# Kernel optimization log

Measured on AMD Instinct MI355X. Metric: run time of the kernel, lower is better.

Reference implementation:

```python
import jax, jax.numpy as jnp
import numpy as np

EMBED_DIM = 1024
NUM_HEADS = 16
SCALE = (EMBED_DIM // NUM_HEADS) ** -0.5  # 0.125


def setup_inputs() -> dict:
    key = jax.random.key(0)
    ks = jax.random.split(key, 9)
    B, S, E = 4, 2048, EMBED_DIM
    std = E ** -0.5
    x = jax.random.normal(ks[0], (B, S, E), dtype=jnp.float32)
    Wq = jax.random.normal(ks[1], (E, E), dtype=jnp.float32) * std
    bq = jax.random.normal(ks[2], (E,), dtype=jnp.float32) * 0.01
    Wk = jax.random.normal(ks[3], (E, E), dtype=jnp.float32) * std
    bk = jax.random.normal(ks[4], (E,), dtype=jnp.float32) * 0.01
    Wv = jax.random.normal(ks[5], (E, E), dtype=jnp.float32) * std
    bv = jax.random.normal(ks[6], (E,), dtype=jnp.float32) * 0.01
    Wo = jax.random.normal(ks[7], (E, E), dtype=jnp.float32) * std
    bo = jax.random.normal(ks[8], (E,), dtype=jnp.float32) * 0.01
    return {"x": x, "Wq": Wq, "bq": bq, "Wk": Wk, "bk": bk,
            "Wv": Wv, "bv": bv, "Wo": Wo, "bo": bo}


def reference(x, Wq, bq, Wk, bk, Wv, bv, Wo, bo):
    # torch nn.Linear: y = x @ W.T + b
    q = jnp.einsum('bse,fe->bsf', x, Wq) + bq   # [B,S,E]
    k = jnp.einsum('bse,fe->bsf', x, Wk) + bk
    v = jnp.einsum('bse,fe->bsf', x, Wv) + bv
    # Bilinear (no softmax) attention: scores = (Q K^T) * scale
    scores = jnp.einsum('bse,bte->bst', q, k) * SCALE  # [B,S,S]
    out = jnp.einsum('bst,bte->bse', scores, v)        # [B,S,E]
    return jnp.einsum('bse,fe->bsf', out, Wo) + bo
```

## Files before the change

### kernel.cpp

```cpp
#include <hip/hip_runtime.h>
#include <stdint.h>

typedef __bf16 bf16_t;
typedef __bf16 bf16x8 __attribute__((ext_vector_type(8)));
typedef __bf16 bf16x4 __attribute__((ext_vector_type(4)));
typedef float floatx4 __attribute__((ext_vector_type(4)));

__device__ __forceinline__ void async_copy16(const bf16_t* g, bf16_t* l) {
  __builtin_amdgcn_global_load_lds(
      (const __attribute__((address_space(1))) void*)g,
      (__attribute__((address_space(3))) void*)l, 16, 0, 0);
}

struct CvtSeg { const float* s; bf16_t* d; long n; };
struct CvtArgs { CvtSeg seg[5]; };

__global__ void cvt_multi(CvtArgs a) {
  CvtSeg sg = a.seg[blockIdx.y];
#pragma unroll
  for (int it = 0; it < 4; it++) {
    long i = (((long)blockIdx.x + (long)it * 2048) * 256 + threadIdx.x) * 4;
    if (i < sg.n) {
      float4 f = *(const float4*)(sg.s + i);
      bf16x4 o;
      o[0] = (bf16_t)f.x; o[1] = (bf16_t)f.y; o[2] = (bf16_t)f.z; o[3] = (bf16_t)f.w;
      *(bf16x4*)(sg.d + i) = o;
    }
  }
}

__global__ __launch_bounds__(256, 2) void qkv3(
    const bf16_t* __restrict__ xb,
    const bf16_t* __restrict__ Wq, const bf16_t* __restrict__ Wk, const bf16_t* __restrict__ Wv,
    const float* __restrict__ bq, const float* __restrict__ bk, const float* __restrict__ bv,
    bf16_t* __restrict__ qout, bf16_t* __restrict__ kT, bf16_t* __restrict__ vT) {
  __shared__ bf16_t As[2 * 4096];
  __shared__ bf16_t Bsh[3][2 * 4096];
  const int L = blockIdx.x;
  const int V = (L & 7) * 64 + (L >> 3);
  const int batch = V >> 7;
  const int rr_   = V & 127;
  const int n0 = (rr_ & 7) * 128;
  const int m0 = (rr_ >> 3) * 128;

  const int tid = threadIdx.x, lane = tid & 63, w = tid >> 6;
  const int wr = w >> 1, wc = w & 1, quad = lane >> 4, lm = lane & 15;
  const int ar = lane >> 2;
  const int ak = (((lane & 3) ^ ((ar >> 1) & 3))) * 8;
  const int swz = (lm >> 1) & 3;

  const bf16_t* ag0 = xb + (long)batch * (2048L * 1024) + (long)(m0 + w * 16 + ar) * 1024 + ak;
  const bf16_t* ag1 = ag0 + 64L * 1024;
  const bf16_t* Wp[3] = {Wq, Wk, Wv};
  const bf16_t* bg0[3];
  const bf16_t* bg1[3];
#pragma unroll
  for (int p = 0; p < 3; p++) {
    bg0[p] = Wp[p] + (long)(n0 + w * 16 + ar) * 1024 + ak;
    bg1[p] = bg0[p] + 64L * 1024;
  }

  floatx4 acc[3][4][4];
#pragma unroll
  for (int p = 0; p < 3; p++)
#pragma unroll
    for (int r = 0; r < 4; r++)
#pragma unroll
      for (int c = 0; c < 4; c++)
        acc[p][r][c] = (floatx4){0.f, 0.f, 0.f, 0.f};

  {
    bf16_t* la = As + w * 512;
    async_copy16(ag0, la);
    async_copy16(ag1, la + 2048);
#pragma unroll
    for (int p = 0; p < 3; p++) {
      bf16_t* lb = Bsh[p] + w * 512;
      async_copy16(bg0[p], lb);
      async_copy16(bg1[p], lb + 2048);
    }
  }
  for (int i = 0; i < 32; i++) {
    __syncthreads();
    if (i + 1 < 32) {
      const int buf = (i + 1) & 1, k0 = (i + 1) * 32;
      bf16_t* la = As + buf * 4096 + w * 512;
      async_copy16(ag0 + k0, la);
      async_copy16(ag1 + k0, la + 2048);
#pragma unroll
      for (int p = 0; p < 3; p++) {
        bf16_t* lb = Bsh[p] + buf * 4096 + w * 512;
        async_copy16(bg0[p] + k0, lb);
        async_copy16(bg1[p] + k0, lb + 2048);
      }
    }
    const bf16_t* Ar = As + (i & 1) * 4096;
    bf16x8 afr[4];
#pragma unroll
    for (int r = 0; r < 4; r++)
      afr[r] = *(const bf16x8*)&Ar[(wr * 64 + r * 16 + lm) * 32 + (quad ^ swz) * 8];
#pragma unroll
    for (int p = 0; p < 3; p++) {
      const bf16_t* Br = Bsh[p] + (i & 1) * 4096;
      bf16x8 bfr[4];
#pragma unroll
      for (int c = 0; c < 4; c++)
        bfr[c] = *(const bf16x8*)&Br[(wc * 64 + c * 16 + lm) * 32 + (quad ^ swz) * 8];
#pragma unroll
      for (int r = 0; r < 4; r++)
#pragma unroll
        for (int c = 0; c < 4; c++)
          acc[p][r][c] = __builtin_amdgcn_mfma_f32_16x16x32_bf16(afr[r], bfr[c], acc[p][r][c], 0, 0, 0);
    }
  }

  const int rowBase = m0 + wr * 64, colBase = n0 + wc * 64;
  {
    bf16_t* C = qout + (long)batch * (2048L * 1024);
#pragma unroll
    for (int r = 0; r < 4; r++) {
      const int row = rowBase + r * 16 + quad * 4;
#pragma unroll
      for (int c = 0; c < 4; c++) {
        const int col = colBase + c * 16 + lm;
        const float bv_ = bq[col];
#pragma unroll
        for (int i = 0; i < 4; i++)
          C[(long)(row + i) * 1024 + col] = (bf16_t)(acc[0][r][c][i] + bv_);
      }
    }
  }
#pragma unroll
  for (int p = 1; p < 3; p++) {
    bf16_t* C = ((p == 1) ? kT : vT) + (long)batch * (1024L * 2048);
    const float* bias = (p == 1) ? bk : bv;
#pragma unroll
    for (int r = 0; r < 4; r++) {
      const int row = rowBase + r * 16 + quad * 4;
#pragma unroll
      for (int c = 0; c < 4; c++) {
        const int col = colBase + c * 16 + lm;
        const float bv_ = bias[col];
        bf16x4 pk;
#pragma unroll
        for (int i = 0; i < 4; i++) pk[i] = (bf16_t)(acc[p][r][c][i] + bv_);
        *(bf16x4*)(C + (long)col * 2048 + row) = pk;
      }
    }
  }
}

template<int OUT_MODE, bool HAS_BIAS, int TOTAL, int BPZ>
__global__ __launch_bounds__(256) void gemm_wp(
    const bf16_t* __restrict__ A, const bf16_t* __restrict__ B,
    void* __restrict__ C, const float* __restrict__ bias,
    int lda, int ldb, int nk, long sA, long sB, long sC, int ldc, float alpha) {
  __shared__ bf16_t Ls[4 * 8192];
  const int L = blockIdx.x;
  const int V = (L & 7) * (TOTAL / 8) + (L >> 3);
  const int batch = V / BPZ;
  const int r_ = V % BPZ;
  const int n0 = (r_ & 7) * 128;
  const int m0 = (r_ >> 3) * 128;

  const int tid = threadIdx.x, lane = tid & 63, w = tid >> 6;
  const int wr = w >> 1, wc = w & 1, quad = lane >> 4, lm = lane & 15;
  const int ar = lane >> 2;
  const int ak = (((lane & 3) ^ ((ar >> 1) & 3))) * 8;
  const int swz = (lm >> 1) & 3;

  bf16_t* Lw = Ls + w * 8192;
  const bf16_t* Ab = A + (long)batch * sA;
  const bf16_t* Bb = B + (long)batch * sB;
  const bf16_t* agA = Ab + (long)(m0 + wr * 64 + ar) * lda + ak;
  const bf16_t* agB = Bb + (long)(n0 + wc * 64 + ar) * ldb + ak;

  auto STAGE = [&](int t, int b) {
    const int k0 = t * 32;
    bf16_t* d = Lw + b * 4096;
#pragma unroll
    for (int j = 0; j < 4; j++)
      async_copy16(agA + (long)j * 16 * lda + k0, d + j * 512);
#pragma unroll
    for (int j = 0; j < 4; j++)
      async_copy16(agB + (long)j * 16 * ldb + k0, d + 2048 + j * 512);
  };

  floatx4 acc[4][4];
#pragma unroll
  for (int r = 0; r < 4; r++)
#pragma unroll
    for (int c = 0; c < 4; c++) acc[r][c] = (floatx4){0.f, 0.f, 0.f, 0.f};

  STAGE(0, 0);
  for (int i = 0; i < nk; i++) {
    if (i + 1 < nk) {
      STAGE(i + 1, (i + 1) & 1);
      asm volatile("s_waitcnt vmcnt(8)" ::: "memory");
    } else {
      asm volatile("s_waitcnt vmcnt(0)" ::: "memory");
    }
    const bf16_t* Aw = Lw + (i & 1) * 4096;
    const bf16_t* Bw = Aw + 2048;
    bf16x8 afr[4], bfr[4];
#pragma unroll
    for (int r = 0; r < 4; r++)
      afr[r] = *(const bf16x8*)&Aw[(r * 16 + lm) * 32 + (quad ^ swz) * 8];
#pragma unroll
    for (int c = 0; c < 4; c++)
      bfr[c] = *(const bf16x8*)&Bw[(c * 16 + lm) * 32 + (quad ^ swz) * 8];
#pragma unroll
    for (int r = 0; r < 4; r++)
#pragma unroll
      for (int c = 0; c < 4; c++)
        acc[r][c] = __builtin_amdgcn_mfma_f32_16x16x32_bf16(afr[r], bfr[c], acc[r][c], 0, 0, 0);
  }

  const int rowBase = m0 + wr * 64, colBase = n0 + wc * 64;
  if (OUT_MODE == 0) {
    bf16_t* Cb = (bf16_t*)C + (long)batch * sC;
#pragma unroll
    for (int r = 0; r < 4; r++) {
      const int row = rowBase + r * 16 + quad * 4;
#pragma unroll
      for (int c = 0; c < 4; c++) {
        const int col = colBase + c * 16 + lm;
        const float bv_ = HAS_BIAS ? bias[col] : 0.f;
#pragma unroll
        for (int i = 0; i < 4; i++)
          Cb[(long)(row + i) * ldc + col] = (bf16_t)(acc[r][c][i] * alpha + bv_);
      }
    }
  } else {
    float* Cf = (float*)C + (long)batch * sC;
#pragma unroll
    for (int r = 0; r < 4; r++) {
      const int row = rowBase + r * 16 + quad * 4;
#pragma unroll
      for (int c = 0; c < 4; c++) {
        const int col = colBase + c * 16 + lm;
        const float bv_ = HAS_BIAS ? bias[col] : 0.f;
#pragma unroll
        for (int i = 0; i < 4; i++)
          Cf[(long)(row + i) * ldc + col] = acc[r][c][i] * alpha + bv_;
      }
    }
  }
}

extern "C" void kernel_launch(void* const* d_in, const int* in_sizes, int n_in,
                              void* d_out, int out_size, void* d_ws, size_t ws_size,
                              hipStream_t stream) {
  const float* x  = (const float*)d_in[0];
  const float* Wq = (const float*)d_in[1];
  const float* bq = (const float*)d_in[2];
  const float* Wk = (const float*)d_in[3];
  const float* bk = (const float*)d_in[4];
  const float* Wv = (const float*)d_in[5];
  const float* bv = (const float*)d_in[6];
  const float* Wo = (const float*)d_in[7];
  const float* bo = (const float*)d_in[8];
  float* out = (float*)d_out;

  const long NX = 8192L * 1024;
  const long NW = 1024L * 1024;

  bf16_t* ws  = (bf16_t*)d_ws;
  bf16_t* xb  = ws;
  bf16_t* Wqb = xb + NX;
  bf16_t* Wkb = Wqb + NW;
  bf16_t* Wvb = Wkb + NW;
  bf16_t* Wob = Wvb + NW;
  bf16_t* qb  = Wob + NW;
  bf16_t* kT  = qb + NX;
  bf16_t* vT  = kT + NX;
  bf16_t* MtTb = xb;
  bf16_t* Gb   = vT;

  CvtArgs ca;
  ca.seg[0] = {x,  xb,  NX};
  ca.seg[1] = {Wq, Wqb, NW};
  ca.seg[2] = {Wk, Wkb, NW};
  ca.seg[3] = {Wv, Wvb, NW};
  ca.seg[4] = {Wo, Wob, NW};
  cvt_multi<<<dim3(2048, 5), 256, 0, stream>>>(ca);

  qkv3<<<dim3(512), 256, 0, stream>>>(xb, Wqb, Wkb, Wvb, bq, bk, bv, qb, kT, vT);

  gemm_wp<0, false, 256, 64><<<dim3(256), 256, 0, stream>>>(
      kT, vT, MtTb, nullptr, 2048, 2048, 64,
      1024L * 2048, 1024L * 2048, 1024L * 1024, 1024, 0.125f);

  gemm_wp<0, false, 256, 64><<<dim3(256), 256, 0, stream>>>(
      Wob, MtTb, Gb, nullptr, 1024, 1024, 32,
      0L, 1024L * 1024, 1024L * 1024, 1024, 1.0f);

  gemm_wp<2, true, 512, 128><<<dim3(512), 256, 0, stream>>>(
      qb, Gb, out, bo, 1024, 1024, 32,
      2048L * 1024, 1024L * 1024, 2048L * 1024, 1024, 1.0f);
}
```

Measured before the change: 231.7 us.

## Fuse three tail GEMMs into one persistent kernel with grid-wide atomic barriers

Replaces the three separate GEMM launches (K^T V, Wo·M, Q·G) with a single persistent 256-block kernel that runs each stage as a tile loop and separates the stages with atomic-counter grid barriers. The barrier counters are zeroed by the conversion kernel. The aim is to remove two kernel launch gaps and the tail idle time between dependent GEMMs. In exchange it relies on all 256 blocks being co-resident and adds spin-wait barrier overhead. The last stage now runs two tiles per block instead of using 512 blocks, and the shared memory allocation grows.

Result: slower. 275.5 us (+18.9%).

```diff
diff --git a/kernel.cpp b/kernel.cpp
--- a/kernel.cpp
+++ b/kernel.cpp
@@ -13,9 +13,11 @@
 }
 
 struct CvtSeg { const float* s; bf16_t* d; long n; };
-struct CvtArgs { CvtSeg seg[5]; };
+struct CvtArgs { CvtSeg seg[5]; unsigned* sync; };
 
 __global__ void cvt_multi(CvtArgs a) {
+  if (blockIdx.x == 0 && blockIdx.y == 0 && threadIdx.x < 8)
+    a.sync[threadIdx.x] = 0u;
   CvtSeg sg = a.seg[blockIdx.y];
 #pragma unroll
   for (int it = 0; it < 4; it++) {
@@ -150,30 +152,13 @@
   }
 }
 
-template<int OUT_MODE, bool HAS_BIAS, int TOTAL, int BPZ>
-__global__ __launch_bounds__(256) void gemm_wp(
-    const bf16_t* __restrict__ A, const bf16_t* __restrict__ B,
-    void* __restrict__ C, const float* __restrict__ bias,
-    int lda, int ldb, int nk, long sA, long sB, long sC, int ldc, float alpha) {
-  __shared__ bf16_t Ls[4 * 8192];
-  const int L = blockIdx.x;
-  const int V = (L & 7) * (TOTAL / 8) + (L >> 3);
-  const int batch = V / BPZ;
-  const int r_ = V % BPZ;
-  const int n0 = (r_ & 7) * 128;
-  const int m0 = (r_ >> 3) * 128;
-
-  const int tid = threadIdx.x, lane = tid & 63, w = tid >> 6;
-  const int wr = w >> 1, wc = w & 1, quad = lane >> 4, lm = lane & 15;
-  const int ar = lane >> 2;
-  const int ak = (((lane & 3) ^ ((ar >> 1) & 3))) * 8;
-  const int swz = (lm >> 1) & 3;
-
-  bf16_t* Lw = Ls + w * 8192;
-  const bf16_t* Ab = A + (long)batch * sA;
-  const bf16_t* Bb = B + (long)batch * sB;
-  const bf16_t* agA = Ab + (long)(m0 + wr * 64 + ar) * lda + ak;
-  const bf16_t* agB = Bb + (long)(n0 + wc * 64 + ar) * ldb + ak;
+template<bool F32OUT, bool HAS_BIAS>
+__device__ __forceinline__ void gemm_tile(
+    bf16_t* Lw, const bf16_t* Ag, const bf16_t* Bg, void* Cb, const float* bias,
+    int m0, int n0, int lda, int ldb, int nk, int ldc, float alpha,
+    int wr, int wc, int quad, int lm, int ar, int ak, int swz) {
+  const bf16_t* agA = Ag + (long)(m0 + wr * 64 + ar) * lda + ak;
+  const bf16_t* agB = Bg + (long)(n0 + wc * 64 + ar) * ldb + ak;
 
   auto STAGE = [&](int t, int b) {
     const int k0 = t * 32;
@@ -217,8 +202,8 @@
   }
 
   const int rowBase = m0 + wr * 64, colBase = n0 + wc * 64;
-  if (OUT_MODE == 0) {
-    bf16_t* Cb = (bf16_t*)C + (long)batch * sC;
+  if (!F32OUT) {
+    bf16_t* Cp = (bf16_t*)Cb;
 #pragma unroll
     for (int r = 0; r < 4; r++) {
       const int row = rowBase + r * 16 + quad * 4;
@@ -228,11 +213,11 @@
         const float bv_ = HAS_BIAS ? bias[col] : 0.f;
 #pragma unroll
         for (int i = 0; i < 4; i++)
-          Cb[(long)(row + i) * ldc + col] = (bf16_t)(acc[r][c][i] * alpha + bv_);
+          Cp[(long)(row + i) * ldc + col] = (bf16_t)(acc[r][c][i] * alpha + bv_);
       }
     }
   } else {
-    float* Cf = (float*)C + (long)batch * sC;
+    float* Cp = (float*)Cb;
 #pragma unroll
     for (int r = 0; r < 4; r++) {
       const int row = rowBase + r * 16 + quad * 4;
@@ -242,9 +227,70 @@
         const float bv_ = HAS_BIAS ? bias[col] : 0.f;
 #pragma unroll
         for (int i = 0; i < 4; i++)
-          Cf[(long)(row + i) * ldc + col] = acc[r][c][i] * alpha + bv_;
-      }
-    }
+          Cp[(long)(row + i) * ldc + col] = acc[r][c][i] * alpha + bv_;
+      }
+    }
+  }
+  asm volatile("s_waitcnt vmcnt(0)" ::: "memory");
+}
+
+__global__ __launch_bounds__(256) void tail3(
+    const bf16_t* __restrict__ kT, const bf16_t* __restrict__ vT,
+    bf16_t* __restrict__ MtTb, bf16_t* __restrict__ Gb,
+    const bf16_t* __restrict__ qb, const bf16_t* __restrict__ Wob,
+    float* __restrict__ out, const float* __restrict__ bo,
+    unsigned* __restrict__ sync) {
+  __shared__ bf16_t Ls[49152];
+  const int L = blockIdx.x;
+  const int V = (L & 7) * 32 + (L >> 3);
+
+  const int tid = threadIdx.x, lane = tid & 63, w = tid >> 6;
+  const int wr = w >> 1, wc = w & 1, quad = lane >> 4, lm = lane & 15;
+  const int ar = lane >> 2;
+  const int ak = (((lane & 3) ^ ((ar >> 1) & 3))) * 8;
+  const int swz = (lm >> 1) & 3;
+  bf16_t* Lw = Ls + w * 8192;
+
+  auto gsync = [&](unsigned* c) {
+    asm volatile("s_waitcnt vmcnt(0)" ::: "memory");
+    __syncthreads();
+    if (tid == 0) {
+      __hip_atomic_fetch_add(c, 1u, __ATOMIC_RELEASE, __HIP_MEMORY_SCOPE_AGENT);
+      while (__hip_atomic_load(c, __ATOMIC_ACQUIRE, __HIP_MEMORY_SCOPE_AGENT) < 256u)
+        __builtin_amdgcn_s_sleep(2);
+    }
+    __syncthreads();
+  };
+
+  {
+    const int batch = V >> 6, r_ = V & 63;
+    const int n0 = (r_ & 7) * 128, m0 = (r_ >> 3) * 128;
+    gemm_tile<false, false>(Lw,
+        kT + (long)batch * (1024L * 2048), vT + (long)batch * (1024L * 2048),
+        MtTb + (long)batch * (1024L * 1024), nullptr,
+        m0, n0, 2048, 2048, 64, 1024, 0.125f, wr, wc, quad, lm, ar, ak, swz);
+  }
+  gsync(sync + 0);
+
+  {
+    const int batch = V >> 6, r_ = V & 63;
+    const int n0 = (r_ & 7) * 128, m0 = (r_ >> 3) * 128;
+    gemm_tile<false, false>(Lw,
+        Wob, MtTb + (long)batch * (1024L * 1024),
+        Gb + (long)batch * (1024L * 1024), nullptr,
+        m0, n0, 1024, 1024, 32, 1024, 1.0f, wr, wc, quad, lm, ar, ak, swz);
+  }
+  gsync(sync + 1);
+
+#pragma unroll
+  for (int half = 0; half < 2; half++) {
+    const int t = V + half * 256;
+    const int batch = t >> 7, r_ = t & 127;
+    const int n0 = (r_ & 7) * 128, m0 = (r_ >> 3) * 128;
+    gemm_tile<true, true>(Lw,
+        qb + (long)batch * (2048L * 1024), Gb + (long)batch * (1024L * 1024),
+        out + (long)batch * (2048L * 1024), bo,
+        m0, n0, 1024, 1024, 32, 1024, 1.0f, wr, wc, quad, lm, ar, ak, swz);
   }
 }
 
@@ -275,7 +321,8 @@
   bf16_t* kT  = qb + NX;
   bf16_t* vT  = kT + NX;
   bf16_t* MtTb = xb;
-  bf16_t* Gb   = vT;
+  bf16_t* Gb   = xb + 4 * NW;
+  unsigned* sync = (unsigned*)(ws + 36L * 1024 * 1024);
 
   CvtArgs ca;
   ca.seg[0] = {x,  xb,  NX};
@@ -283,19 +330,10 @@
   ca.seg[2] = {Wk, Wkb, NW};
   ca.seg[3] = {Wv, Wvb, NW};
   ca.seg[4] = {Wo, Wob, NW};
+  ca.sync = sync;
   cvt_multi<<<dim3(2048, 5), 256, 0, stream>>>(ca);
 
   qkv3<<<dim3(512), 256, 0, stream>>>(xb, Wqb, Wkb, Wvb, bq, bk, bv, qb, kT, vT);
 
-  gemm_wp<0, false, 256, 64><<<dim3(256), 256, 0, stream>>>(
-      kT, vT, MtTb, nullptr, 2048, 2048, 64,
-      1024L * 2048, 1024L * 2048, 1024L * 1024, 1024, 0.125f);
-
-  gemm_wp<0, false, 256, 64><<<dim3(256), 256, 0, stream>>>(
-      Wob, MtTb, Gb, nullptr, 1024, 1024, 32,
-      0L, 1024L * 1024, 1024L * 1024, 1024, 1.0f);
-
-  gemm_wp<2, true, 512, 128><<<dim3(512), 256, 0, stream>>>(
-      qb, Gb, out, bo, 1024, 1024, 32,
-      2048L * 1024, 1024L * 1024, 2048L * 1024, 1024, 1.0f);
-}
+  tail3<<<dim3(256), 256, 0, stream>>>(kT, vT, MtTb, Gb, qb, Wob, out, bo, sync);
+}
```

## Share block-wide LDS tiles across waves with K=64 stages in GEMM kernel

Applied to the files above, without the earlier changes.

The GEMM kernel used to give each wave its own private copy of its A and B tiles in LDS. It now cooperatively stages a shared 128x64 A tile and B tile per block, so the duplicate global loads disappear. Each stage covers a K depth of 64 (two sub-tiles of 32), so the loop runs half as many iterations, and the launch trip counts are halved to match. In exchange, a block-wide __syncthreads per iteration replaces the per-wave vmcnt waits, and launch_bounds asks for 2 blocks per CU.

Result: no change. 234.8 us (+1.3%).

```diff
diff --git a/kernel.cpp b/kernel.cpp
--- a/kernel.cpp
+++ b/kernel.cpp
@@ -151,11 +151,12 @@
 }
 
 template<int OUT_MODE, bool HAS_BIAS, int TOTAL, int BPZ>
-__global__ __launch_bounds__(256) void gemm_wp(
+__global__ __launch_bounds__(256, 2) void gemm64(
     const bf16_t* __restrict__ A, const bf16_t* __restrict__ B,
     void* __restrict__ C, const float* __restrict__ bias,
     int lda, int ldb, int nk, long sA, long sB, long sC, int ldc, float alpha) {
-  __shared__ bf16_t Ls[4 * 8192];
+  __shared__ bf16_t As[2][2][4096];
+  __shared__ bf16_t Bs[2][2][4096];
   const int L = blockIdx.x;
   const int V = (L & 7) * (TOTAL / 8) + (L >> 3);
   const int batch = V / BPZ;
@@ -169,21 +170,23 @@
   const int ak = (((lane & 3) ^ ((ar >> 1) & 3))) * 8;
   const int swz = (lm >> 1) & 3;
 
-  bf16_t* Lw = Ls + w * 8192;
   const bf16_t* Ab = A + (long)batch * sA;
   const bf16_t* Bb = B + (long)batch * sB;
-  const bf16_t* agA = Ab + (long)(m0 + wr * 64 + ar) * lda + ak;
-  const bf16_t* agB = Bb + (long)(n0 + wc * 64 + ar) * ldb + ak;
-
-  auto STAGE = [&](int t, int b) {
-    const int k0 = t * 32;
-    bf16_t* d = Lw + b * 4096;
-#pragma unroll
-    for (int j = 0; j < 4; j++)
-      async_copy16(agA + (long)j * 16 * lda + k0, d + j * 512);
-#pragma unroll
-    for (int j = 0; j < 4; j++)
-      async_copy16(agB + (long)j * 16 * ldb + k0, d + 2048 + j * 512);
+  const bf16_t* ag0 = Ab + (long)(m0 + w * 16 + ar) * lda + ak;
+  const bf16_t* ag1 = ag0 + (long)64 * lda;
+  const bf16_t* bg0 = Bb + (long)(n0 + w * 16 + ar) * ldb + ak;
+  const bf16_t* bg1 = bg0 + (long)64 * ldb;
+
+  auto STAGE = [&](int t, int buf) {
+    const int k0 = t * 64;
+#pragma unroll
+    for (int p = 0; p < 2; p++) {
+      const int kp = k0 + p * 32;
+      async_copy16(ag0 + kp, &As[buf][p][w * 512]);
+      async_copy16(ag1 + kp, &As[buf][p][w * 512 + 2048]);
+      async_copy16(bg0 + kp, &Bs[buf][p][w * 512]);
+      async_copy16(bg1 + kp, &Bs[buf][p][w * 512 + 2048]);
+    }
   };
 
   floatx4 acc[4][4];
@@ -194,26 +197,24 @@
 
   STAGE(0, 0);
   for (int i = 0; i < nk; i++) {
-    if (i + 1 < nk) {
-      STAGE(i + 1, (i + 1) & 1);
-      asm volatile("s_waitcnt vmcnt(8)" ::: "memory");
-    } else {
-      asm volatile("s_waitcnt vmcnt(0)" ::: "memory");
-    }
-    const bf16_t* Aw = Lw + (i & 1) * 4096;
-    const bf16_t* Bw = Aw + 2048;
-    bf16x8 afr[4], bfr[4];
-#pragma unroll
-    for (int r = 0; r < 4; r++)
-      afr[r] = *(const bf16x8*)&Aw[(r * 16 + lm) * 32 + (quad ^ swz) * 8];
-#pragma unroll
-    for (int c = 0; c < 4; c++)
-      bfr[c] = *(const bf16x8*)&Bw[(c * 16 + lm) * 32 + (quad ^ swz) * 8];
-#pragma unroll
-    for (int r = 0; r < 4; r++)
+    __syncthreads();
+    if (i + 1 < nk) STAGE(i + 1, (i + 1) & 1);
+    const int cb = i & 1;
+#pragma unroll
+    for (int p = 0; p < 2; p++) {
+      bf16x8 afr[4], bfr[4];
+#pragma unroll
+      for (int r = 0; r < 4; r++)
+        afr[r] = *(const bf16x8*)&As[cb][p][(wr * 64 + r * 16 + lm) * 32 + (quad ^ swz) * 8];
 #pragma unroll
       for (int c = 0; c < 4; c++)
-        acc[r][c] = __builtin_amdgcn_mfma_f32_16x16x32_bf16(afr[r], bfr[c], acc[r][c], 0, 0, 0);
+        bfr[c] = *(const bf16x8*)&Bs[cb][p][(wc * 64 + c * 16 + lm) * 32 + (quad ^ swz) * 8];
+#pragma unroll
+      for (int r = 0; r < 4; r++)
+#pragma unroll
+        for (int c = 0; c < 4; c++)
+          acc[r][c] = __builtin_amdgcn_mfma_f32_16x16x32_bf16(afr[r], bfr[c], acc[r][c], 0, 0, 0);
+    }
   }
 
   const int rowBase = m0 + wr * 64, colBase = n0 + wc * 64;
@@ -287,15 +288,15 @@
 
   qkv3<<<dim3(512), 256, 0, stream>>>(xb, Wqb, Wkb, Wvb, bq, bk, bv, qb, kT, vT);
 
-  gemm_wp<0, false, 256, 64><<<dim3(256), 256, 0, stream>>>(
-      kT, vT, MtTb, nullptr, 2048, 2048, 64,
+  gemm64<0, false, 256, 64><<<dim3(256), 256, 0, stream>>>(
+      kT, vT, MtTb, nullptr, 2048, 2048, 32,
       1024L * 2048, 1024L * 2048, 1024L * 1024, 1024, 0.125f);
 
-  gemm_wp<0, false, 256, 64><<<dim3(256), 256, 0, stream>>>(
-      Wob, MtTb, Gb, nullptr, 1024, 1024, 32,
+  gemm64<0, false, 256, 64><<<dim3(256), 256, 0, stream>>>(
+      Wob, MtTb, Gb, nullptr, 1024, 1024, 16,
       0L, 1024L * 1024, 1024L * 1024, 1024, 1.0f);
 
-  gemm_wp<2, true, 512, 128><<<dim3(512), 256, 0, stream>>>(
-      qb, Gb, out, bo, 1024, 1024, 32,
+  gemm64<2, true, 512, 128><<<dim3(512), 256, 0, stream>>>(
+      qb, Gb, out, bo, 1024, 1024, 16,
       2048L * 1024, 1024L * 1024, 2048L * 1024, 1024, 1.0f);
 }
```
